# Optimization experiments

Hardware: AMD Instinct MI355X
Metric: run time of the kernel (lower is better)

## Reference

```python
import math
import jax, jax.numpy as jnp
import numpy as np
from jax import lax

EPS = 1e-6
SAMPLE_RATIO = 0.25
K = 5


def _grid_idx(loc_orig, h, w):
    # loc_orig in [-1,1] -> nearest grid cell flat index (row-major)
    loc = (jnp.clip(loc_orig, -1.0, 1.0) + 1.0) * 0.5
    col = jnp.clip(jnp.round(loc[..., 0] * (w - 1)).astype(jnp.int32), 0, w - 1)
    row = jnp.clip(jnp.round(loc[..., 1] * (h - 1)).astype(jnp.int32), 0, h - 1)
    return row * w + col


def token2map(x, loc_orig, idx_agg, H, W):
    # scatter tokens (via their original points) into an HxW grid, averaging per cell
    B, N, C = x.shape
    N0 = idx_agg.shape[1]
    idx_hw = _grid_idx(loc_orig, H, W)                      # (B, N0)
    tok = jax.vmap(lambda xb, ib: xb[ib])(x, idx_agg)       # (B, N0, C)

    def per_b(ihw, t):
        cnt = jax.ops.segment_sum(jnp.ones((N0,), x.dtype), ihw, num_segments=H * W)
        s = jax.ops.segment_sum(t, ihw, num_segments=H * W)
        return s / (cnt + EPS)[:, None]

    grid = jax.vmap(per_b)(idx_hw, tok)                     # (B, H*W, C)
    return grid.reshape(B, H, W, C).transpose(0, 3, 1, 2)   # (B, C, H, W)


def map2token(x_map, N, loc_orig, idx_agg, agg_weight):
    # gather map values at original points, weighted scatter-reduce back to N tokens
    B, C, h, w = x_map.shape
    idx_hw = _grid_idx(loc_orig, h, w)
    flat = x_map.reshape(B, C, h * w).transpose(0, 2, 1)    # (B, hw, C)
    feat = jax.vmap(lambda fb, ib: fb[ib])(flat, idx_hw)    # (B, N0, C)
    aw = agg_weight[..., 0]                                 # (B, N0)

    def per_b(ia, a, f):
        tot = jax.ops.segment_sum(a, ia, num_segments=N) + EPS
        return jax.ops.segment_sum(f * (a / tot[ia])[:, None], ia, num_segments=N)

    return jax.vmap(per_b)(idx_agg, aw, feat)               # (B, N, C)


def cluster_dpc_knn(x, cluster_num, k):
    # DPC-KNN: density from k-NN distances, parent distance, score = dist*density
    B, N, C = x.shape
    sq = jnp.sum(x * x, -1)
    dist = jnp.sqrt(jnp.maximum(sq[:, :, None] + sq[:, None, :]
                                - 2.0 * jnp.einsum('bnc,bmc->bnm', x, x), 0.0)) / math.sqrt(C)
    neg_near, _ = lax.top_k(-dist, k)                       # k nearest (incl. self, dist 0)
    density = jnp.exp(-jnp.mean(jnp.square(neg_near), -1))  # (B, N)
    mask = density[:, None, :] > density[:, :, None]
    dist_max = jnp.max(dist.reshape(B, -1), -1)[:, None, None]
    d_parent = jnp.min(jnp.where(mask, dist, dist_max), -1)
    score = d_parent * density
    _, index_down = lax.top_k(score, cluster_num)           # (B, M) cluster centers
    dist_down = jax.vmap(lambda db, ib: db[ib])(dist, index_down)  # (B, M, N)
    idx_cluster = jnp.argmin(dist_down, axis=1)             # (B, N)
    b = jnp.arange(B)[:, None]
    idx_cluster = idx_cluster.at[b, index_down].set(jnp.arange(cluster_num)[None, :])
    return idx_cluster


def layer_norm(x, g, b):
    mu = jnp.mean(x, -1, keepdims=True)
    xc = x - mu
    return xc * lax.rsqrt(jnp.mean(xc * xc, -1, keepdims=True) + 1e-5) * g + b


def setup_inputs() -> dict:
    key = jax.random.key(0)
    ks = jax.random.split(key, 8)
    B, N, C, DOUT, H, W = 4, 4096, 128, 256, 64, 64
    return {
        "x": jax.random.normal(ks[0], (B, N, C), jnp.float32),
        "loc_orig": jax.random.uniform(ks[1], (B, N, 2), jnp.float32, minval=-1.0, maxval=1.0),
        "idx_agg": jax.random.randint(ks[2], (B, N), 0, N),
        "agg_weight": jax.random.uniform(ks[3], (B, N, 1), jnp.float32),
        "H": H,
        "W": W,
        "idx_k_loc": jax.random.randint(ks[4], (B, N, K), 0, N),
        "conv_w": jax.random.normal(ks[5], (DOUT, C, 3, 3), jnp.float32) * 0.02,
        "conv_b": jnp.zeros((DOUT,), jnp.float32),
        "skip_w": jax.random.normal(ks[6], (DOUT, C), jnp.float32) * 0.02,
        "ln_g": jnp.ones((DOUT,), jnp.float32),
        "ln_b": jnp.zeros((DOUT,), jnp.float32),
        "conf_w": jax.random.normal(ks[7], (1, DOUT), jnp.float32) * 0.02,
        "conf_b": jnp.zeros((1,), jnp.float32),
    }


def reference(x, loc_orig, idx_agg, agg_weight, H, W, idx_k_loc,
              conv_w, conv_b, skip_w, ln_g, ln_b, conf_w, conf_b):
    B, N, C = x.shape
    x_map = token2map(x, loc_orig, idx_agg, H, W)           # (B, C, H, W)
    x_map = lax.conv_general_dilated(x_map, conv_w, (2, 2), ((1, 1), (1, 1)),
                                     dimension_numbers=('NCHW', 'OIHW', 'NCHW'))
    x_map = x_map + conv_b[None, :, None, None]             # (B, DOUT, H/2, W/2)
    xt = map2token(x_map, N, loc_orig, idx_agg, agg_weight) + x @ skip_w.T
    xt = layer_norm(xt, ln_g, ln_b)
    conf = xt @ conf_w.T + conf_b                           # (B, N, 1)
    weight = jnp.exp(conf)[..., 0]                          # (B, N)
    M = max(int(math.ceil(N * SAMPLE_RATIO)), 1)
    idx_cluster = cluster_dpc_knn(xt, M, K)                 # (B, N)

    def merge_b(ic, wb, xb):
        allw = jax.ops.segment_sum(wb, ic, num_segments=M) + EPS
        nw = wb / allw[ic]
        return jax.ops.segment_sum(xb * nw[:, None], ic, num_segments=M), nw

    x_down, norm_w = jax.vmap(merge_b)(idx_cluster, weight, xt)   # (B, M, DOUT), (B, N)
    idx_agg_down = jax.vmap(lambda ic, ia: ic[ia])(idx_cluster, idx_agg)        # (B, N0)
    weight_t = jax.vmap(lambda nw, ia: nw[ia])(norm_w, idx_agg)[..., None]      # (B, N0, 1)
    agg_weight_down = agg_weight * weight_t
    agg_weight_down = agg_weight_down / jnp.max(agg_weight_down, axis=1, keepdims=True)
    # down_block treated as identity (external module); use_grid=False path -> idx_k_loc_down is None
    return (x_down, idx_agg_down, agg_weight_down)
```

## Files before the change

kernel.cpp:

```cpp
#include <hip/hip_runtime.h>
#include <math.h>

#define NB 4
#define NT 4096
#define CI 128
#define DOUT 256
#define HWI 4096
#define HWO 1024
#define MC 1024
#define EPS_F 1e-6f
#define GSZ 16777216ull
#define GSZB 67108864ull

typedef unsigned short u16;
typedef __attribute__((ext_vector_type(8))) short bf16x8;
typedef __attribute__((ext_vector_type(4))) float f32x4;

static const size_t OFF_XMAP  = 0;
static const size_t OFF_CNT   = OFF_XMAP + 8388608;
static const size_t OFF_TOT   = OFF_CNT  + 65536;
static const size_t OFF_ALLW  = OFF_TOT  + 65536;
static const size_t OFF_VMAX  = OFF_ALLW + 16384;
static const size_t OFF_AWDM  = OFF_VMAX + 256;
static const size_t ZERO_BYTES= OFF_AWDM + 256;
static const size_t OFF_YMAP  = ZERO_BYTES;
static const size_t OFF_XT    = OFF_YMAP + 4194304;
static const size_t OFF_SQ    = OFF_XT + 16777216;
static const size_t OFF_DEN   = OFF_SQ + 65536;
static const size_t OFF_SCORE = OFF_DEN + 65536;
static const size_t OFF_WT    = OFF_SCORE + 65536;
static const size_t OFF_AWD   = OFF_WT + 65536;
static const size_t OFF_IDXD  = OFF_AWD + 65536;
static const size_t OFF_IDXC  = OFF_IDXD + 16384;
static const size_t OFF_INV   = OFF_IDXC + 65536;
static const size_t OFF_WTR   = OFF_INV + 65536;
static const size_t OFF_SWT   = OFF_WTR + 1179648;
static const size_t OFF_P     = OFF_SWT + 131072;
static const size_t OFF_XH    = OFF_P + 18874368;
static const size_t OFF_XM    = OFF_XH + 8388608;
static const size_t OFF_XL    = OFF_XM + 8388608;
static const size_t OFF_G     = OFF_XL + 8388608;
static const size_t DPSTRIDE  = (size_t)NT*32*6;

__device__ __forceinline__ float waveSum(float v){
#pragma unroll
  for (int m = 1; m < 64; m <<= 1) v += __shfl_xor(v, m, 64);
  return v;
}
__device__ __forceinline__ float blockSum256(float v, float* red){
  v = waveSum(v);
  int lane = threadIdx.x & 63, wid = threadIdx.x >> 6;
  __syncthreads();
  if (lane == 0) red[wid] = v;
  __syncthreads();
  return red[0] + red[1] + red[2] + red[3];
}
__device__ __forceinline__ void merge5(float& a0, float& a1, float& a2, float& a3, float& a4,
                                       float b0, float b1, float b2, float b3, float b4){
  float l0=a0,l1=a1,l2=a2,l3=fminf(a3,b4),l4=fminf(a4,b3),l5=b2,l6=b1,l7=b0;
  float t0=fminf(l0,l4), t4=fmaxf(l0,l4);
  float t1=fminf(l1,l5), t5=fmaxf(l1,l5);
  float t2=fminf(l2,l6), t6=fmaxf(l2,l6);
  float t3=fminf(l3,l7), t7=fmaxf(l3,l7);
  float u0=fminf(t0,t2), u2=fmaxf(t0,t2);
  float u1=fminf(t1,t3), u3=fmaxf(t1,t3);
  float u4=fminf(t4,t6);
  float u5=fminf(t5,t7);
  a0=fminf(u0,u1); a1=fmaxf(u0,u1);
  a2=fminf(u2,u3); a3=fmaxf(u2,u3);
  a4=fminf(u4,u5);
}
__device__ __forceinline__ void ins5(float v, float& t0, float& t1, float& t2, float& t3, float& t4){
  t4 = fminf(t4, v);
  float a;
  a = fminf(t3,t4); t4 = fmaxf(t3,t4); t3 = a;
  a = fminf(t2,t3); t3 = fmaxf(t2,t3); t2 = a;
  a = fminf(t1,t2); t2 = fmaxf(t1,t2); t1 = a;
  a = fminf(t0,t1); t1 = fmaxf(t0,t1); t0 = a;
}
__device__ __forceinline__ int grid_cell(float lx, float ly, int dim){
  lx = (fminf(fmaxf(lx, -1.f), 1.f) + 1.f) * 0.5f;
  ly = (fminf(fmaxf(ly, -1.f), 1.f) + 1.f) * 0.5f;
  float s = (float)(dim - 1);
  int col = (int)rintf(lx * s); col = min(max(col, 0), dim - 1);
  int row = (int)rintf(ly * s); row = min(max(row, 0), dim - 1);
  return row * dim + col;
}

__global__ __launch_bounds__(256) void t2m_scatter(const float* __restrict__ x,
                                                   const float* __restrict__ loc,
                                                   const int* __restrict__ idx_agg,
                                                   const float* __restrict__ aggw,
                                                   float* __restrict__ xmap, float* __restrict__ cnt,
                                                   float* __restrict__ tot){
  int lin = blockIdx.x * 256 + threadIdx.x;
// ... 128 lines not shown
  atomicAdd(&xt[((size_t)(b*NT + ia))*DOUT + d], val);
}

__global__ __launch_bounds__(256) void ln_kernel(float* __restrict__ xt,
                                                 const float* __restrict__ g,
                                                 const float* __restrict__ bta,
                                                 const float* __restrict__ cw,
                                                 const float* __restrict__ cb,
                                                 float* __restrict__ sq, float* __restrict__ wt){
  __shared__ float red[4];
  int row = blockIdx.x;
  int d = threadIdx.x;
  float v = xt[(size_t)row*DOUT + d];
  float mu = blockSum256(v, red) * (1.0f/256.0f);
  float xc = v - mu;
  float var = blockSum256(xc*xc, red) * (1.0f/256.0f);
  float rn = 1.0f / sqrtf(var + 1e-5f);
  float y = xc * rn * g[d] + bta[d];
  xt[(size_t)row*DOUT + d] = y;
  float s2 = blockSum256(y*y, red);
  float cf = blockSum256(y*cw[d], red);
  if (d == 0){ sq[row] = s2; wt[row] = expf(cf + cb[0]); }
}

__global__ __launch_bounds__(256) void xsplit_kernel(const float* __restrict__ xt,
                                                     u16* __restrict__ xh,
                                                     u16* __restrict__ xm,
                                                     u16* __restrict__ xl){
  int idx = blockIdx.x*256 + threadIdx.x;
  float2 v = *(const float2*)(xt + (size_t)idx*2);
  unsigned ph, pm, pl;
  {
    unsigned u = __float_as_uint(v.x);
    unsigned h0 = u >> 16;
    float r1 = v.x - __uint_as_float(u & 0xFFFF0000u);
    unsigned u1 = __float_as_uint(r1);
    unsigned m0 = u1 >> 16;
    float r2 = r1 - __uint_as_float(u1 & 0xFFFF0000u);
    unsigned l0 = __float_as_uint(r2) >> 16;
    unsigned u2 = __float_as_uint(v.y);
    unsigned h1 = u2 >> 16;
    float s1 = v.y - __uint_as_float(u2 & 0xFFFF0000u);
    unsigned u3 = __float_as_uint(s1);
    unsigned m1 = u3 >> 16;
    float s2 = s1 - __uint_as_float(u3 & 0xFFFF0000u);
    unsigned l1 = __float_as_uint(s2) >> 16;
    ph = h0 | (h1 << 16); pm = m0 | (m1 << 16); pl = l0 | (l1 << 16);
  }
  *(unsigned*)(xh + (size_t)idx*2) = ph;
  *(unsigned*)(xm + (size_t)idx*2) = pm;
  *(unsigned*)(xl + (size_t)idx*2) = pl;
}

__global__ __launch_bounds__(256) void gram_mfma(const u16* __restrict__ xh,
                                                 const u16* __restrict__ xm,
                                                 const u16* __restrict__ xl,
                                                 const float* __restrict__ sq,
                                                 float* __restrict__ G,
                                                 float* __restrict__ Dpart,
                                                 int b_base, size_t gstride){
  __shared__ u16 usmem[24576];
  u16* Au = usmem;
  u16* Bu = usmem + 12288;
  int b = b_base + blockIdx.y;
  float* Gb = G + (size_t)blockIdx.y*gstride;
  float* Dp = Dpart + (size_t)blockIdx.y*DPSTRIDE;
  int t = blockIdx.x;
  int ti = 0, accu = 0;
  while (accu + ti + 1 <= t){ accu += ti + 1; ++ti; }
  int tj = t - accu;
  int i0 = ti*128, j0 = tj*128;
  int tid = threadIdx.x;
  int w = tid >> 6, l = tid & 63;
  int lrow = l & 15, lg = l >> 4;
  int li = tid & 127, kq = tid >> 7;
  const size_t base = (size_t)b*NT*256;
  size_t arow = base + (size_t)(i0 + li)*256 + kq*16;
  size_t brow = base + (size_t)(j0 + li)*256 + kq*16;
  const u16* csrc[3] = {xh, xm, xl};
  int ga0 = ((li*4 + kq*2 + 0) ^ (li & 7)) * 8;
  int ga1 = ((li*4 + kq*2 + 1) ^ (li & 7)) * 8;
  f32x4 acc[2][8];
  f32x4 z; z[0]=0.f; z[1]=0.f; z[2]=0.f; z[3]=0.f;
#pragma unroll
  for (int mr = 0; mr < 2; ++mr)
#pragma unroll
    for (int n0 = 0; n0 < 8; ++n0) acc[mr][n0] = z;
  for (int kc = 0; kc < 8; ++kc){
    int k0 = kc*32;
    __syncthreads();
#pragma unroll
    for (int c = 0; c < 3; ++c){
      const u16* s = csrc[c];
      bf16x8 a0 = *(const bf16x8*)(s + arow + k0);
      bf16x8 a1 = *(const bf16x8*)(s + arow + k0 + 8);
      bf16x8 b0 = *(const bf16x8*)(s + brow + k0);
      bf16x8 b1 = *(const bf16x8*)(s + brow + k0 + 8);
      *(bf16x8*)(Au + c*4096 + ga0) = a0;
      *(bf16x8*)(Au + c*4096 + ga1) = a1;
      *(bf16x8*)(Bu + c*4096 + ga0) = b0;
      *(bf16x8*)(Bu + c*4096 + ga1) = b1;
    }
    __syncthreads();
    bf16x8 af[2][3];
#pragma unroll
    for (int mr = 0; mr < 2; ++mr){
      int row = w*32 + mr*16 + lrow;
      int off = ((row*4 + lg) ^ (row & 7)) * 8;
#pragma unroll
      for (int c = 0; c < 3; ++c)
        af[mr][c] = *(const bf16x8*)(Au + c*4096 + off);
    }
#pragma unroll
    for (int n0 = 0; n0 < 8; ++n0){
      int rowb = n0*16 + lrow;
      int offb = ((rowb*4 + lg) ^ (rowb & 7)) * 8;
      bf16x8 bh = *(const bf16x8*)(Bu + 0*4096 + offb);
      bf16x8 bm = *(const bf16x8*)(Bu + 1*4096 + offb);
      bf16x8 bl = *(const bf16x8*)(Bu + 2*4096 + offb);
#pragma unroll
      for (int mr = 0; mr < 2; ++mr){
        acc[mr][n0] = __builtin_amdgcn_mfma_f32_16x16x32_bf16(af[mr][0], bh, acc[mr][n0], 0, 0, 0);
        acc[mr][n0] = __builtin_amdgcn_mfma_f32_16x16x32_bf16(af[mr][0], bm, acc[mr][n0], 0, 0, 0);
        acc[mr][n0] = __builtin_amdgcn_mfma_f32_16x16x32_bf16(af[mr][1], bh, acc[mr][n0], 0, 0, 0);
        acc[mr][n0] = __builtin_amdgcn_mfma_f32_16x16x32_bf16(af[mr][1], bm, acc[mr][n0], 0, 0, 0);
        acc[mr][n0] = __builtin_amdgcn_mfma_f32_16x16x32_bf16(af[mr][0], bl, acc[mr][n0], 0, 0, 0);
        acc[mr][n0] = __builtin_amdgcn_mfma_f32_16x16x32_bf16(af[mr][2], bh, acc[mr][n0], 0, 0, 0);
      }
    }
  }
  const float* sqb2 = sq + b*NT;
  {
    float sqj_c[8];
#pragma unroll
    for (int n0 = 0; n0 < 8; ++n0) sqj_c[n0] = sqb2[j0 + n0*16 + lrow];
#pragma unroll
    for (int mr = 0; mr < 2; ++mr)
#pragma unroll
      for (int r = 0; r < 4; ++r){
        int row = i0 + w*32 + mr*16 + lg*4 + r;
        float sqi_v = sqb2[row];
        float t0=INFINITY,t1=INFINITY,t2=INFINITY,t3=INFINITY,t4=INFINITY;
        float mx = 0.f;
#pragma unroll
        for (int n0 = 0; n0 < 8; ++n0){
          float v = fmaxf(sqi_v + sqj_c[n0] - 2.0f*acc[mr][n0][r], 0.0f);
          mx = fmaxf(mx, v);
          ins5(v,t0,t1,t2,t3,t4);
        }
#pragma unroll
        for (int m = 1; m < 16; m <<= 1){
          float b0=__shfl_xor(t0,m,64), b1=__shfl_xor(t1,m,64), b2=__shfl_xor(t2,m,64),
                b3=__shfl_xor(t3,m,64), b4=__shfl_xor(t4,m,64);
          merge5(t0,t1,t2,t3,t4,b0,b1,b2,b3,b4);
          mx = fmaxf(mx, __shfl_xor(mx,m,64));
        }
        if (lrow == 0){
          float* dpp = Dp + ((size_t)row*32 + tj)*6;
          dpp[0]=t0; dpp[1]=t1; dpp[2]=t2; dpp[3]=t3; dpp[4]=t4; dpp[5]=mx;
        }
      }
  }
#pragma unroll
  for (int mr = 0; mr < 2; ++mr)
#pragma unroll
    for (int n0 = 0; n0 < 8; ++n0)
#pragma unroll
      for (int r = 0; r < 4; ++r)
        Gb[(size_t)(i0 + w*32 + mr*16 + lg*4 + r)*NT + j0 + n0*16 + lrow] = acc[mr][n0][r];
  if (ti != tj){
    float* T = (float*)usmem;
    int q = tid >> 3, u = tid & 7;
    float sqi_u[16];
#pragma unroll
    for (int e = 0; e < 16; ++e) sqi_u[e] = sqb2[i0 + u*16 + e];
#pragma unroll
    for (int cc = 0; cc < 4; ++cc){
      __syncthreads();
#pragma unroll
      for (int nn = 0; nn < 2; ++nn){
        int n0 = cc*2 + nn;
#pragma unroll
        for (int mr = 0; mr < 2; ++mr)
#pragma unroll
          for (int r = 0; r < 4; ++r)
            T[(nn*16 + lrow)*129 + w*32 + mr*16 + lg*4 + r] = acc[mr][n0][r];
      }
      __syncthreads();
      const float* Trow = &T[q*129 + u*16];
      float* dst = Gb + (size_t)(j0 + cc*32 + q)*NT + i0 + u*16;
      float gv[16];
#pragma unroll
      for (int e = 0; e < 16; ++e) gv[e] = Trow[e];
      float4 o0, o1, o2, o3;
      o0.x=gv[0]; o0.y=gv[1]; o0.z=gv[2]; o0.w=gv[3];
      o1.x=gv[4]; o1.y=gv[5]; o1.z=gv[6]; o1.w=gv[7];
      o2.x=gv[8]; o2.y=gv[9]; o2.z=gv[10]; o2.w=gv[11];
      o3.x=gv[12]; o3.y=gv[13]; o3.z=gv[14]; o3.w=gv[15];
      *(float4*)dst = o0; *(float4*)(dst + 4) = o1;
      *(float4*)(dst + 8) = o2; *(float4*)(dst + 12) = o3;
      {
        int jr = j0 + cc*32 + q;
        float sqj_m = sqb2[jr];
        float t0=INFINITY,t1=INFINITY,t2=INFINITY,t3=INFINITY,t4=INFINITY;
        float mx = 0.f;
#pragma unroll
        for (int e = 0; e < 16; ++e){
          float v = fmaxf(sqj_m + sqi_u[e] - 2.0f*gv[e], 0.0f);
          mx = fmaxf(mx, v);
          ins5(v,t0,t1,t2,t3,t4);
        }
#pragma unroll
        for (int m = 1; m < 8; m <<= 1){
          float b0=__shfl_xor(t0,m,64), b1=__shfl_xor(t1,m,64), b2=__shfl_xor(t2,m,64),
                b3=__shfl_xor(t3,m,64), b4=__shfl_xor(t4,m,64);
          merge5(t0,t1,t2,t3,t4,b0,b1,b2,b3,b4);
          mx = fmaxf(mx, __shfl_xor(mx,m,64));
        }
        if (u == 0){
          float* dpp = Dp + ((size_t)jr*32 + ti)*6;
          dpp[0]=t0; dpp[1]=t1; dpp[2]=t2; dpp[3]=t3; dpp[4]=t4; dpp[5]=mx;
        }
      }
    }
  }
}

__global__ __launch_bounds__(256) void dens_merge(const float* __restrict__ Dpart,
                                                  float* __restrict__ density, int* __restrict__ vmax,
                                                  int b_base){
  int b = b_base + blockIdx.y;
  const float* Dp = Dpart + (size_t)blockIdx.y*DPSTRIDE;
  int row = blockIdx.x*256 + threadIdx.x;
  const float* p = Dp + (size_t)row*32*6;
  float t0=INFINITY,t1=INFINITY,t2=INFINITY,t3=INFINITY,t4=INFINITY;
  float mx = 0.f;
#pragma unroll 4
  for (int tt = 0; tt < 32; ++tt){
    merge5(t0,t1,t2,t3,t4, p[tt*6+0], p[tt*6+1], p[tt*6+2], p[tt*6+3], p[tt*6+4]);
    mx = fmaxf(mx, p[tt*6+5]);
  }
  float d0=sqrtf(t0)*0.0625f, d1=sqrtf(t1)*0.0625f, d2=sqrtf(t2)*0.0625f,
        d3=sqrtf(t3)*0.0625f, d4=sqrtf(t4)*0.0625f;
  float s = d0*d0; s += d1*d1; s += d2*d2; s += d3*d3; s += d4*d4;
  density[b*NT + row] = expf(-(s / 5.0f));
#pragma unroll
  for (int m = 1; m < 64; m <<= 1) mx = fmaxf(mx, __shfl_xor(mx, m, 64));
  if ((threadIdx.x & 63) == 0) atomicMax(vmax + b, __float_as_int(mx));
}

__global__ __launch_bounds__(256) void parent_all(const float* __restrict__ G, size_t gstride,
                                                  const float* __restrict__ sq,
                                                  const float* __restrict__ density, const int* __restrict__ vmax,
                                                  float* __restrict__ score, int b_base){
  int b = b_base + blockIdx.y;
  const float* Gb = G + (size_t)blockIdx.y*gstride;
  int i = blockIdx.x*4 + (threadIdx.x >> 6);
  int lane = threadIdx.x & 63;
  const float* sqb = sq + b*NT;
  const float* den = density + b*NT;
  float sqi = sqb[i];
  float di = den[i];
  const float4* row4 = (const float4*)(Gb + (size_t)i*NT);
  const float4* sq4  = (const float4*)sqb;
  const float4* dn4  = (const float4*)den;
  float4 ga[8], gb2[8];
#pragma unroll
  for (int p = 0; p < 8; ++p) ga[p] = row4[p*64 + lane];
#pragma unroll
  for (int p = 0; p < 8; ++p) gb2[p] = row4[(8+p)*64 + lane];
  float minv = INFINITY;
#pragma unroll
  for (int p = 0; p < 8; ++p){
    float4 g4 = ga[p];
    float4 s4 = sq4[p*64 + lane];
    float4 d4 = dn4[p*64 + lane];
    float v0 = fmaxf(sqi + s4.x - 2.0f*g4.x, 0.0f);
    float v1 = fmaxf(sqi + s4.y - 2.0f*g4.y, 0.0f);
    float v2 = fmaxf(sqi + s4.z - 2.0f*g4.z, 0.0f);
    float v3 = fmaxf(sqi + s4.w - 2.0f*g4.w, 0.0f);
    minv = fminf(minv, (d4.x > di) ? v0 : INFINITY);
    minv = fminf(minv, (d4.y > di) ? v1 : INFINITY);
    minv = fminf(minv, (d4.z > di) ? v2 : INFINITY);
    minv = fminf(minv, (d4.w > di) ? v3 : INFINITY);
  }
#pragma unroll
  for (int p = 0; p < 8; ++p){
    float4 g4 = gb2[p];
    float4 s4 = sq4[(8+p)*64 + lane];
    float4 d4 = dn4[(8+p)*64 + lane];
    float v0 = fmaxf(sqi + s4.x - 2.0f*g4.x, 0.0f);
    float v1 = fmaxf(sqi + s4.y - 2.0f*g4.y, 0.0f);
    float v2 = fmaxf(sqi + s4.z - 2.0f*g4.z, 0.0f);
    float v3 = fmaxf(sqi + s4.w - 2.0f*g4.w, 0.0f);
    minv = fminf(minv, (d4.x > di) ? v0 : INFINITY);
    minv = fminf(minv, (d4.y > di) ? v1 : INFINITY);
    minv = fminf(minv, (d4.z > di) ? v2 : INFINITY);
    minv = fminf(minv, (d4.w > di) ? v3 : INFINITY);
  }
#pragma unroll
  for (int m = 1; m < 64; m <<= 1) minv = fminf(minv, __shfl_xor(minv,m,64));
  if (lane == 0){
    float dmax = sqrtf(__int_as_float(vmax[b])) * 0.0625f;
    float dp = isinf(minv) ? dmax : sqrtf(minv) * 0.0625f;
    score[b*NT + i] = dp * di;
  }
}

__device__ __forceinline__ bool kv_lt(float s1, int a1, float s2, int a2){
  return (s1 > s2) || (s1 == s2 && a1 < a2);
}
#define KV_CMPX(sx,ax,sy,ay,up) do{ bool _l = kv_lt(sx,ax,sy,ay); \
  if (_l != (up)) { float _ts=sx; sx=sy; sy=_ts; int _ta=ax; ax=ay; ay=_ta; } }while(0)
#define KV_TAKE(sx,ax,ps,pa,eqd) do{ bool _keep = kv_lt(sx,ax,ps,pa) == (eqd); \
  if(!_keep){ sx=(ps); ax=(pa); } }while(0)

__global__ __launch_bounds__(1024) void topk_all(const float* __restrict__ score, int* __restrict__ idx_down,
                                                 int* __restrict__ inv, int b_base){
  __shared__ float ss[4096];
  __shared__ int ii[4096];
  int b = b_base + blockIdx.x;
  int t = threadIdx.x;
  float s0,s1,s2,s3; int a0,a1,a2,a3;
  {
    float4 v = *(const float4*)(score + b*NT + 4*t);
    s0=v.x; s1=v.y; s2=v.z; s3=v.w;
    a0=4*t; a1=4*t+1; a2=4*t+2; a3=4*t+3;
    int4 mi; mi.x=-1; mi.y=-1; mi.z=-1; mi.w=-1;
    *(int4*)(inv + b*NT + 4*t) = mi;
  }
  for (int k = 2; k <= 4096; k <<= 1){
    bool upT = ((4*t) & k) == 0;
    for (int j = k >> 1; j >= 256; j >>= 1){
      __syncthreads();
      float4 sv; sv.x=s0; sv.y=s1; sv.z=s2; sv.w=s3;
      int4 av; av.x=a0; av.y=a1; av.z=a2; av.w=a3;
      *(float4*)&ss[4*t] = sv;
      *(int4*)&ii[4*t] = av;
      __syncthreads();
      int pt = t ^ (j >> 2);
      bool eqd = ((t & (j >> 2)) == 0) == upT;
      float4 ps = *(const float4*)&ss[4*pt];
      int4  pa = *(const int4*)&ii[4*pt];
      KV_TAKE(s0,a0,ps.x,pa.x,eqd);
      KV_TAKE(s1,a1,ps.y,pa.y,eqd);
      KV_TAKE(s2,a2,ps.z,pa.z,eqd);
      KV_TAKE(s3,a3,ps.w,pa.w,eqd);
    }
    int jhi = (k >> 1) < 128 ? (k >> 1) : 128;
    for (int j = jhi; j >= 4; j >>= 1){
      int dl = j >> 2;
      bool eqd = ((t & dl) == 0) == upT;
      { float ps=__shfl_xor(s0,dl,64); int pa=__shfl_xor(a0,dl,64); KV_TAKE(s0,a0,ps,pa,eqd); }
      { float ps=__shfl_xor(s1,dl,64); int pa=__shfl_xor(a1,dl,64); KV_TAKE(s1,a1,ps,pa,eqd); }
      { float ps=__shfl_xor(s2,dl,64); int pa=__shfl_xor(a2,dl,64); KV_TAKE(s2,a2,ps,pa,eqd); }
      { float ps=__shfl_xor(s3,dl,64); int pa=__shfl_xor(a3,dl,64); KV_TAKE(s3,a3,ps,pa,eqd); }
    }
    if (k >= 4){
      KV_CMPX(s0,a0,s2,a2,upT);
      KV_CMPX(s1,a1,s3,a3,upT);
      KV_CMPX(s0,a0,s1,a1,upT);
      KV_CMPX(s2,a2,s3,a3,upT);
    } else {
      KV_CMPX(s0,a0,s1,a1,true);
      KV_CMPX(s2,a2,s3,a3,false);
    }
  }
  __syncthreads();
  if (t < 256){
    idx_down[b*MC + 4*t + 0] = a0; inv[b*NT + a0] = 4*t + 0;
    idx_down[b*MC + 4*t + 1] = a1; inv[b*NT + a1] = 4*t + 1;
    idx_down[b*MC + 4*t + 2] = a2; inv[b*NT + a2] = 4*t + 2;
    idx_down[b*MC + 4*t + 3] = a3; inv[b*NT + a3] = 4*t + 3;
  }
}

__global__ __launch_bounds__(256) void assign_all(const float* __restrict__ G, size_t gstride,
                                                  const float* __restrict__ sq,
                                                  const int* __restrict__ idx_down, const int* __restrict__ inv,
                                                  const float* __restrict__ wt,
                                                  int* __restrict__ idx_cluster, float* __restrict__ allw,
                                                  int b_base){
  int b = b_base + blockIdx.y;
  const float* Gb = G + (size_t)blockIdx.y*gstride;
  int jl = threadIdx.x & 15, mq = threadIdx.x >> 4;
  int j = blockIdx.x * 16 + jl;
  const float* sqb = sq + b*NT;
  float sqj = sqb[j];
  const int* idb = idx_down + b*MC;
  float bestd = INFINITY; int bestm = 0x7fffffff;
  for (int m = mq*64; m < mq*64 + 64; ++m){
    int im = idb[m];
    float g = Gb[(size_t)im*NT + j];
    float v = fmaxf(sqb[im] + sqj - 2.0f*g, 0.0f);
    float d = sqrtf(v) * 0.0625f;
    if (d < bestd){ bestd = d; bestm = m; }
  }
  __shared__ float ld[16][17];
  __shared__ int lm[16][17];
  ld[mq][jl] = bestd; lm[mq][jl] = bestm;
  __syncthreads();
  if (mq == 0){
    for (int q = 1; q < 16; ++q){
      float d2 = ld[q][jl]; int m2 = lm[q][jl];
      if (d2 < bestd || (d2 == bestd && m2 < bestm)){ bestd = d2; bestm = m2; }
    }
    int iv = inv[b*NT + j];
    int final_m = (iv >= 0) ? iv : bestm;
    idx_cluster[b*NT + j] = final_m;
    atomicAdd(&allw[b*MC + final_m], wt[b*NT + j]);
  }
}

__global__ __launch_bounds__(256) void xdown_kernel(const int* __restrict__ idx_cluster,
                                                    const float* __restrict__ wt, const float* __restrict__ allw,
                                                    const float* __restrict__ xt, float* __restrict__ out0){
  int bn = blockIdx.x;
  int d = threadIdx.x;
  int b = bn >> 12;
  int ic = idx_cluster[bn];
  float nw = wt[bn] / (allw[b*MC + ic] + EPS_F);
  float v = xt[(size_t)bn*DOUT + d] * nw;
  atomicAdd(&out0[((size_t)(b*MC + ic))*DOUT + d], v);
}
__global__ __launch_bounds__(256) void out12a_kernel(const int* __restrict__ idx_agg, const int* __restrict__ idx_cluster,
                                                     const float* __restrict__ aggw,
                                                     const float* __restrict__ wt, const float* __restrict__ allw,
                                                     float* __restrict__ awd, int* __restrict__ awdmax,
                                                     float* __restrict__ out1){
  __shared__ float red[4];
  int lin = blockIdx.x * 256 + threadIdx.x;
  int b = lin >> 12;
  int ia = idx_agg[lin];
  int ic = idx_cluster[b*NT + ia];
  out1[lin] = (float)ic;
  float nw = wt[b*NT + ia] / (allw[b*MC + ic] + EPS_F);
  float v = aggw[lin] * nw;
  awd[lin] = v;
  float wv = v;
#pragma unroll
  for (int m = 1; m < 64; m <<= 1) wv = fmaxf(wv, __shfl_xor(wv, m, 64));
  int lane = threadIdx.x & 63, wid = threadIdx.x >> 6;
  if (lane == 0) red[wid] = wv;
  __syncthreads();
  if (threadIdx.x == 0){
    float bm = fmaxf(fmaxf(red[0], red[1]), fmaxf(red[2], red[3]));
    atomicMax(&awdmax[b], __float_as_int(bm));
  }
}
__global__ __launch_bounds__(256) void out2_kernel(const float* __restrict__ awd, const int* __restrict__ awdmax,
                                                   float* __restrict__ out2){
  int lin = blockIdx.x * 256 + threadIdx.x;
  int b = lin >> 12;
  out2[lin] = awd[lin] / __int_as_float(awdmax[b]);
}

extern "C" void kernel_launch(void* const* d_in, const int* in_sizes, int n_in,
                              void* d_out, int out_size, void* d_ws, size_t ws_size,
                              hipStream_t stream) {
  const float* x      = (const float*)d_in[0];
  const float* loc    = (const float*)d_in[1];
  const int*   idxagg = (const int*)d_in[2];
  const float* aggw   = (const float*)d_in[3];
  const float* convw  = (const float*)d_in[7];
  const float* convb  = (const float*)d_in[8];
  const float* skipw  = (const float*)d_in[9];
  const float* lng    = (const float*)d_in[10];
  const float* lnb    = (const float*)d_in[11];
  const float* confw  = (const float*)d_in[12];
  const float* confb  = (const float*)d_in[13];

  char* ws = (char*)d_ws;
  float* w_xmap  = (float*)(ws + OFF_XMAP);
  float* w_cnt   = (float*)(ws + OFF_CNT);
  float* w_tot   = (float*)(ws + OFF_TOT);
  float* w_allw  = (float*)(ws + OFF_ALLW);
  int*   w_vmax  = (int*)  (ws + OFF_VMAX);
  int*   w_awdm  = (int*)  (ws + OFF_AWDM);
  float* w_ymap  = (float*)(ws + OFF_YMAP);
  float* w_xt    = (float*)(ws + OFF_XT);
  float* w_sq    = (float*)(ws + OFF_SQ);
  float* w_den   = (float*)(ws + OFF_DEN);
  float* w_score = (float*)(ws + OFF_SCORE);
  float* w_wt    = (float*)(ws + OFF_WT);
  float* w_awd   = (float*)(ws + OFF_AWD);
  int*   w_idxd  = (int*)  (ws + OFF_IDXD);
  int*   w_idxc  = (int*)  (ws + OFF_IDXC);
  int*   w_inv   = (int*)  (ws + OFF_INV);
  float* w_wtr   = (float*)(ws + OFF_WTR);
  float* w_swt   = (float*)(ws + OFF_SWT);
  float* w_p     = (float*)(ws + OFF_P);
  u16*   w_xh    = (u16*)  (ws + OFF_XH);
  u16*   w_xm    = (u16*)  (ws + OFF_XM);
  u16*   w_xl    = (u16*)  (ws + OFF_XL);
  float* w_g     = (float*)(ws + OFF_G);
  float* w_dpart = (float*)(ws + OFF_P);

  int gcount = 1;
  for (int k = 4; k >= 1; --k){
    if (OFF_G + (size_t)k*GSZB <= ws_size){ gcount = k; break; }
  }

  float* out0 = (float*)d_out;
  float* out1 = out0 + NB*MC*DOUT;
  float* out2 = out1 + NB*NT;

  hipMemsetAsync(ws, 0, ZERO_BYTES, stream);
  hipMemsetAsync(out0, 0, (size_t)NB*MC*DOUT*sizeof(float), stream);

  t2m_scatter<<<NB*NT*CI/256, 256, 0, stream>>>(x, loc, idxagg, aggw, w_xmap, w_cnt, w_tot);
  wprep_kernel<<<1280, 256, 0, stream>>>(convw, skipw, w_wtr, w_swt);
  im2col_kernel<<<2048, 256, 0, stream>>>(w_xmap, w_cnt, w_p);
  conv_gemm<<<dim3(64, 8), 256, 0, stream>>>(w_p, w_wtr, convb, w_ymap);
  skip_kernel<<<NB*NT/8, 256, 0, stream>>>(x, w_swt, w_xt);
  m2t_scatter<<<NB*NT, 256, 0, stream>>>(w_ymap, loc, idxagg, aggw, w_tot, w_xt);
  ln_kernel<<<NB*NT, 256, 0, stream>>>(w_xt, lng, lnb, confw, confb, w_sq, w_wt);
  xsplit_kernel<<<NB*NT*DOUT/512, 256, 0, stream>>>(w_xt, w_xh, w_xm, w_xl);

  for (int g0 = 0; g0 < NB; g0 += gcount){
    int gy = (NB - g0 < gcount) ? (NB - g0) : gcount;
    gram_mfma  <<<dim3(528, gy), 256, 0, stream>>>(w_xh, w_xm, w_xl, w_sq, w_g, w_dpart, g0, GSZ);
    dens_merge <<<dim3(16, gy), 256, 0, stream>>>(w_dpart, w_den, w_vmax, g0);
    parent_all <<<dim3(1024, gy), 256, 0, stream>>>(w_g, GSZ, w_sq, w_den, w_vmax, w_score, g0);
    topk_all   <<<gy, 1024, 0, stream>>>(w_score, w_idxd, w_inv, g0);
    assign_all <<<dim3(256, gy), 256, 0, stream>>>(w_g, GSZ, w_sq, w_idxd, w_inv, w_wt, w_idxc, w_allw, g0);
  }

  xdown_kernel<<<NB*NT, 256, 0, stream>>>(w_idxc, w_wt, w_allw, w_xt, out0);
  out12a_kernel<<<NB*NT/256, 256, 0, stream>>>(idxagg, w_idxc, aggw, w_wt, w_allw, w_awd, w_awdm, out1);
  out2_kernel<<<NB*NT/256, 256, 0, stream>>>(w_awd, w_awdm, out2);

  (void)in_sizes; (void)n_in; (void)out_size;
}
```

Before: 635.0 us.

## Recompute Gram tiles via MFMA instead of materializing full distance matrix

Drops the stored 4096x4096 Gram matrix per batch. The parent-distance and cluster-assignment stages now recompute the needed dot products with split-bf16 MFMA tiles and reduce partial minima in small merge kernels. This removes the large writes and re-reads of the Gram matrix and the batch-group loop, and all batches launch in one grid. The cost is running the 3-way split MFMA gram about twice more (full for parent, 1024x4096 for assign).

```diff
diff --git a/kernel.cpp b/kernel.cpp
--- a/kernel.cpp
+++ b/kernel.cpp
@@ -9,8 +9,6 @@
 #define HWO 1024
 #define MC 1024
 #define EPS_F 1e-6f
-#define GSZ 16777216ull
-#define GSZB 67108864ull
 
 typedef unsigned short u16;
 typedef __attribute__((ext_vector_type(8))) short bf16x8;
@@ -39,8 +37,11 @@
 static const size_t OFF_XH    = OFF_P + 18874368;
 static const size_t OFF_XM    = OFF_XH + 8388608;
 static const size_t OFF_XL    = OFF_XM + 8388608;
-static const size_t OFF_G     = OFF_XL + 8388608;
+static const size_t OFF_PP    = OFF_XL + 8388608;
+static const size_t OFF_APD   = OFF_PP + (size_t)NB*NT*32*4;
+static const size_t OFF_APM   = OFF_APD + (size_t)NB*NT*8*4;
 static const size_t DPSTRIDE  = (size_t)NT*32*6;
+static const size_t PPSTRIDE  = (size_t)NT*32;
 
 __device__ __forceinline__ float waveSum(float v){
 #pragma unroll
@@ -275,19 +276,16 @@
   *(unsigned*)(xl + (size_t)idx*2) = pl;
 }
 
-__global__ __launch_bounds__(256) void gram_mfma(const u16* __restrict__ xh,
+__global__ __launch_bounds__(256) void dens_mfma(const u16* __restrict__ xh,
                                                  const u16* __restrict__ xm,
                                                  const u16* __restrict__ xl,
                                                  const float* __restrict__ sq,
-                                                 float* __restrict__ G,
-                                                 float* __restrict__ Dpart,
-                                                 int b_base, size_t gstride){
+                                                 float* __restrict__ Dpart){
   __shared__ u16 usmem[24576];
   u16* Au = usmem;
   u16* Bu = usmem + 12288;
-  int b = b_base + blockIdx.y;
-  float* Gb = G + (size_t)blockIdx.y*gstride;
-  float* Dp = Dpart + (size_t)blockIdx.y*DPSTRIDE;
+  int b = blockIdx.y;
+  float* Dp = Dpart + (size_t)b*DPSTRIDE;
   int t = blockIdx.x;
   int ti = 0, accu = 0;
   while (accu + ti + 1 <= t){ accu += ti + 1; ++ti; }
@@ -384,13 +382,6 @@
         }
       }
   }
-#pragma unroll
-  for (int mr = 0; mr < 2; ++mr)
-#pragma unroll
-    for (int n0 = 0; n0 < 8; ++n0)
-#pragma unroll
-      for (int r = 0; r < 4; ++r)
-        Gb[(size_t)(i0 + w*32 + mr*16 + lg*4 + r)*NT + j0 + n0*16 + lrow] = acc[mr][n0][r];
   if (ti != tj){
     float* T = (float*)usmem;
     int q = tid >> 3, u = tid & 7;
@@ -411,49 +402,38 @@
       }
       __syncthreads();
       const float* Trow = &T[q*129 + u*16];
-      float* dst = Gb + (size_t)(j0 + cc*32 + q)*NT + i0 + u*16;
       float gv[16];
 #pragma unroll
       for (int e = 0; e < 16; ++e) gv[e] = Trow[e];
-      float4 o0, o1, o2, o3;
-      o0.x=gv[0]; o0.y=gv[1]; o0.z=gv[2]; o0.w=gv[3];
-      o1.x=gv[4]; o1.y=gv[5]; o1.z=gv[6]; o1.w=gv[7];
-      o2.x=gv[8]; o2.y=gv[9]; o2.z=gv[10]; o2.w=gv[11];
-      o3.x=gv[12]; o3.y=gv[13]; o3.z=gv[14]; o3.w=gv[15];
-      *(float4*)dst = o0; *(float4*)(dst + 4) = o1;
-      *(float4*)(dst + 8) = o2; *(float4*)(dst + 12) = o3;
-      {
-        int jr = j0 + cc*32 + q;
-        float sqj_m = sqb2[jr];
-        float t0=INFINITY,t1=INFINITY,t2=INFINITY,t3=INFINITY,t4=INFINITY;
-        float mx = 0.f;
-#pragma unroll
-        for (int e = 0; e < 16; ++e){
-          float v = fmaxf(sqj_m + sqi_u[e] - 2.0f*gv[e], 0.0f);
-          mx = fmaxf(mx, v);
-          ins5(v,t0,t1,t2,t3,t4);
-        }
-#pragma unroll
-        for (int m = 1; m < 8; m <<= 1){
-          float b0=__shfl_xor(t0,m,64), b1=__shfl_xor(t1,m,64), b2=__shfl_xor(t2,m,64),
-                b3=__shfl_xor(t3,m,64), b4=__shfl_xor(t4,m,64);
-          merge5(t0,t1,t2,t3,t4,b0,b1,b2,b3,b4);
-          mx = fmaxf(mx, __shfl_xor(mx,m,64));
-        }
-        if (u == 0){
-          float* dpp = Dp + ((size_t)jr*32 + ti)*6;
-          dpp[0]=t0; dpp[1]=t1; dpp[2]=t2; dpp[3]=t3; dpp[4]=t4; dpp[5]=mx;
-        }
+      int jr = j0 + cc*32 + q;
+      float sqj_m = sqb2[jr];
+      float t0=INFINITY,t1=INFINITY,t2=INFINITY,t3=INFINITY,t4=INFINITY;
+      float mx = 0.f;
+#pragma unroll
+      for (int e = 0; e < 16; ++e){
+        float v = fmaxf(sqj_m + sqi_u[e] - 2.0f*gv[e], 0.0f);
+        mx = fmaxf(mx, v);
+        ins5(v,t0,t1,t2,t3,t4);
+      }
+#pragma unroll
+      for (int m = 1; m < 8; m <<= 1){
+        float b0=__shfl_xor(t0,m,64), b1=__shfl_xor(t1,m,64), b2=__shfl_xor(t2,m,64),
+              b3=__shfl_xor(t3,m,64), b4=__shfl_xor(t4,m,64);
+        merge5(t0,t1,t2,t3,t4,b0,b1,b2,b3,b4);
+        mx = fmaxf(mx, __shfl_xor(mx,m,64));
+      }
+      if (u == 0){
+        float* dpp = Dp + ((size_t)jr*32 + ti)*6;
+        dpp[0]=t0; dpp[1]=t1; dpp[2]=t2; dpp[3]=t3; dpp[4]=t4; dpp[5]=mx;
       }
     }
   }
 }
 
 __global__ __launch_bounds__(256) void dens_merge(const float* __restrict__ Dpart,
-                                                  float* __restrict__ density, int* __restrict__ vmax,
-                                                  int b_base){
-  int b = b_base + blockIdx.y;
-  const float* Dp = Dpart + (size_t)blockIdx.y*DPSTRIDE;
+                                                  float* __restrict__ density, int* __restrict__ vmax){
+  int b = blockIdx.y;
+  const float* Dp = Dpart + (size_t)b*DPSTRIDE;
   int row = blockIdx.x*256 + threadIdx.x;
   const float* p = Dp + (size_t)row*32*6;
   float t0=INFINITY,t1=INFINITY,t2=INFINITY,t3=INFINITY,t4=INFINITY;
@@ -472,62 +452,160 @@
   if ((threadIdx.x & 63) == 0) atomicMax(vmax + b, __float_as_int(mx));
 }
 
-__global__ __launch_bounds__(256) void parent_all(const float* __restrict__ G, size_t gstride,
-                                                  const float* __restrict__ sq,
-                                                  const float* __restrict__ density, const int* __restrict__ vmax,
-                                                  float* __restrict__ score, int b_base){
-  int b = b_base + blockIdx.y;
-  const float* Gb = G + (size_t)blockIdx.y*gstride;
-  int i = blockIdx.x*4 + (threadIdx.x >> 6);
-  int lane = threadIdx.x & 63;
-  const float* sqb = sq + b*NT;
-  const float* den = density + b*NT;
-  float sqi = sqb[i];
-  float di = den[i];
-  const float4* row4 = (const float4*)(Gb + (size_t)i*NT);
-  const float4* sq4  = (const float4*)sqb;
-  const float4* dn4  = (const float4*)den;
-  float4 ga[8], gb2[8];
-#pragma unroll
-  for (int p = 0; p < 8; ++p) ga[p] = row4[p*64 + lane];
-#pragma unroll
-  for (int p = 0; p < 8; ++p) gb2[p] = row4[(8+p)*64 + lane];
-  float minv = INFINITY;
-#pragma unroll
-  for (int p = 0; p < 8; ++p){
-    float4 g4 = ga[p];
-    float4 s4 = sq4[p*64 + lane];
-    float4 d4 = dn4[p*64 + lane];
-    float v0 = fmaxf(sqi + s4.x - 2.0f*g4.x, 0.0f);
-    float v1 = fmaxf(sqi + s4.y - 2.0f*g4.y, 0.0f);
-    float v2 = fmaxf(sqi + s4.z - 2.0f*g4.z, 0.0f);
-    float v3 = fmaxf(sqi + s4.w - 2.0f*g4.w, 0.0f);
-    minv = fminf(minv, (d4.x > di) ? v0 : INFINITY);
-    minv = fminf(minv, (d4.y > di) ? v1 : INFINITY);
-    minv = fminf(minv, (d4.z > di) ? v2 : INFINITY);
-    minv = fminf(minv, (d4.w > di) ? v3 : INFINITY);
-  }
-#pragma unroll
-  for (int p = 0; p < 8; ++p){
-    float4 g4 = gb2[p];
-    float4 s4 = sq4[(8+p)*64 + lane];
-    float4 d4 = dn4[(8+p)*64 + lane];
-    float v0 = fmaxf(sqi + s4.x - 2.0f*g4.x, 0.0f);
-    float v1 = fmaxf(sqi + s4.y - 2.0f*g4.y, 0.0f);
-    float v2 = fmaxf(sqi + s4.z - 2.0f*g4.z, 0.0f);
-    float v3 = fmaxf(sqi + s4.w - 2.0f*g4.w, 0.0f);
-    minv = fminf(minv, (d4.x > di) ? v0 : INFINITY);
-    minv = fminf(minv, (d4.y > di) ? v1 : INFINITY);
-    minv = fminf(minv, (d4.z > di) ? v2 : INFINITY);
-    minv = fminf(minv, (d4.w > di) ? v3 : INFINITY);
-  }
-#pragma unroll
-  for (int m = 1; m < 64; m <<= 1) minv = fminf(minv, __shfl_xor(minv,m,64));
-  if (lane == 0){
-    float dmax = sqrtf(__int_as_float(vmax[b])) * 0.0625f;
-    float dp = isinf(minv) ? dmax : sqrtf(minv) * 0.0625f;
-    score[b*NT + i] = dp * di;
-  }
+__global__ __launch_bounds__(256) void parent_mfma(const u16* __restrict__ xh,
+                                                   const u16* __restrict__ xm,
+                                                   const u16* __restrict__ xl,
+                                                   const float* __restrict__ sq,
+                                                   const float* __restrict__ den,
+                                                   float* __restrict__ Ppart){
+  __shared__ u16 usmem[24576];
+  u16* Au = usmem;
+  u16* Bu = usmem + 12288;
+  int b = blockIdx.y;
+  float* Pp = Ppart + (size_t)b*PPSTRIDE;
+  int t = blockIdx.x;
+  int ti = 0, accu = 0;
+  while (accu + ti + 1 <= t){ accu += ti + 1; ++ti; }
+  int tj = t - accu;
+  int i0 = ti*128, j0 = tj*128;
+  int tid = threadIdx.x;
+  int w = tid >> 6, l = tid & 63;
+  int lrow = l & 15, lg = l >> 4;
+  int li = tid & 127, kq = tid >> 7;
+  const size_t base = (size_t)b*NT*256;
+  size_t arow = base + (size_t)(i0 + li)*256 + kq*16;
+  size_t brow = base + (size_t)(j0 + li)*256 + kq*16;
+  const u16* csrc[3] = {xh, xm, xl};
+  int ga0 = ((li*4 + kq*2 + 0) ^ (li & 7)) * 8;
+  int ga1 = ((li*4 + kq*2 + 1) ^ (li & 7)) * 8;
+  f32x4 acc[2][8];
+  f32x4 z; z[0]=0.f; z[1]=0.f; z[2]=0.f; z[3]=0.f;
+#pragma unroll
+  for (int mr = 0; mr < 2; ++mr)
+#pragma unroll
+    for (int n0 = 0; n0 < 8; ++n0) acc[mr][n0] = z;
+  for (int kc = 0; kc < 8; ++kc){
+    int k0 = kc*32;
+    __syncthreads();
+#pragma unroll
+    for (int c = 0; c < 3; ++c){
+      const u16* s = csrc[c];
+      bf16x8 a0 = *(const bf16x8*)(s + arow + k0);
+      bf16x8 a1 = *(const bf16x8*)(s + arow + k0 + 8);
+      bf16x8 b0 = *(const bf16x8*)(s + brow + k0);
+      bf16x8 b1 = *(const bf16x8*)(s + brow + k0 + 8);
+      *(bf16x8*)(Au + c*4096 + ga0) = a0;
+      *(bf16x8*)(Au + c*4096 + ga1) = a1;
+      *(bf16x8*)(Bu + c*4096 + ga0) = b0;
+      *(bf16x8*)(Bu + c*4096 + ga1) = b1;
+    }
+    __syncthreads();
+    bf16x8 af[2][3];
+#pragma unroll
+    for (int mr = 0; mr < 2; ++mr){
+      int row = w*32 + mr*16 + lrow;
+      int off = ((row*4 + lg) ^ (row & 7)) * 8;
+#pragma unroll
+      for (int c = 0; c < 3; ++c)
+        af[mr][c] = *(const bf16x8*)(Au + c*4096 + off);
+    }
+#pragma unroll
+    for (int n0 = 0; n0 < 8; ++n0){
+      int rowb = n0*16 + lrow;
+      int offb = ((rowb*4 + lg) ^ (rowb & 7)) * 8;
+      bf16x8 bh = *(const bf16x8*)(Bu + 0*4096 + offb);
+      bf16x8 bm = *(const bf16x8*)(Bu + 1*4096 + offb);
+      bf16x8 bl = *(const bf16x8*)(Bu + 2*4096 + offb);
+#pragma unroll
+      for (int mr = 0; mr < 2; ++mr){
+        acc[mr][n0] = __builtin_amdgcn_mfma_f32_16x16x32_bf16(af[mr][0], bh, acc[mr][n0], 0, 0, 0);
+        acc[mr][n0] = __builtin_amdgcn_mfma_f32_16x16x32_bf16(af[mr][0], bm, acc[mr][n0], 0, 0, 0);
+        acc[mr][n0] = __builtin_amdgcn_mfma_f32_16x16x32_bf16(af[mr][1], bh, acc[mr][n0], 0, 0, 0);
+        acc[mr][n0] = __builtin_amdgcn_mfma_f32_16x16x32_bf16(af[mr][1], bm, acc[mr][n0], 0, 0, 0);
+        acc[mr][n0] = __builtin_amdgcn_mfma_f32_16x16x32_bf16(af[mr][0], bl, acc[mr][n0], 0, 0, 0);
+        acc[mr][n0] = __builtin_amdgcn_mfma_f32_16x16x32_bf16(af[mr][2], bh, acc[mr][n0], 0, 0, 0);
+      }
+    }
+  }
+  const float* sqb2 = sq + b*NT;
+  const float* denb = den + b*NT;
+  {
+    float sqj_c[8], dnj_c[8];
+#pragma unroll
+    for (int n0 = 0; n0 < 8; ++n0){
+      sqj_c[n0] = sqb2[j0 + n0*16 + lrow];
+      dnj_c[n0] = denb[j0 + n0*16 + lrow];
+    }
+#pragma unroll
+    for (int mr = 0; mr < 2; ++mr)
+#pragma unroll
+      for (int r = 0; r < 4; ++r){
+        int row = i0 + w*32 + mr*16 + lg*4 + r;
+        float di = denb[row];
+        float sqi_v = sqb2[row];
+        float mn = INFINITY;
+#pragma unroll
+        for (int n0 = 0; n0 < 8; ++n0){
+          float v = fmaxf(sqi_v + sqj_c[n0] - 2.0f*acc[mr][n0][r], 0.0f);
+          mn = fminf(mn, (dnj_c[n0] > di) ? v : INFINITY);
+        }
+#pragma unroll
+        for (int m = 1; m < 16; m <<= 1) mn = fminf(mn, __shfl_xor(mn, m, 64));
+        if (lrow == 0) Pp[(size_t)row*32 + tj] = mn;
+      }
+  }
+  if (ti != tj){
+    float* T = (float*)usmem;
+    int q = tid >> 3, u = tid & 7;
+    float sqi_u[16], dni_u[16];
+#pragma unroll
+    for (int e = 0; e < 16; ++e){
+      sqi_u[e] = sqb2[i0 + u*16 + e];
+      dni_u[e] = denb[i0 + u*16 + e];
+    }
+#pragma unroll
+    for (int cc = 0; cc < 4; ++cc){
+      __syncthreads();
+#pragma unroll
+      for (int nn = 0; nn < 2; ++nn){
+        int n0 = cc*2 + nn;
+#pragma unroll
+        for (int mr = 0; mr < 2; ++mr)
+#pragma unroll
+          for (int r = 0; r < 4; ++r)
+            T[(nn*16 + lrow)*129 + w*32 + mr*16 + lg*4 + r] = acc[mr][n0][r];
+      }
+      __syncthreads();
+      const float* Trow = &T[q*129 + u*16];
+      int jr = j0 + cc*32 + q;
+      float dj = denb[jr];
+      float sqj_m = sqb2[jr];
+      float mn = INFINITY;
+#pragma unroll
+      for (int e = 0; e < 16; ++e){
+        float v = fmaxf(sqj_m + sqi_u[e] - 2.0f*Trow[e], 0.0f);
+        mn = fminf(mn, (dni_u[e] > dj) ? v : INFINITY);
+      }
+#pragma unroll
+      for (int m = 1; m < 8; m <<= 1) mn = fminf(mn, __shfl_xor(mn, m, 64));
+      if (u == 0) Pp[(size_t)jr*32 + ti] = mn;
+    }
+  }
+}
+
+__global__ __launch_bounds__(256) void parent_merge(const float* __restrict__ Ppart,
+                                                    const float* __restrict__ density,
+                                                    const int* __restrict__ vmax,
+                                                    float* __restrict__ score){
+  int b = blockIdx.y;
+  int row = blockIdx.x*256 + threadIdx.x;
+  const float* p = Ppart + (size_t)b*PPSTRIDE + (size_t)row*32;
+  float mn = INFINITY;
+#pragma unroll 4
+  for (int tt = 0; tt < 32; ++tt) mn = fminf(mn, p[tt]);
+  float dmax = sqrtf(__int_as_float(vmax[b])) * 0.0625f;
+  float dp = isinf(mn) ? dmax : sqrtf(mn) * 0.0625f;
+  score[b*NT + row] = dp * density[b*NT + row];
 }
 
 __device__ __forceinline__ bool kv_lt(float s1, int a1, float s2, int a2){
@@ -539,10 +617,10 @@
   if(!_keep){ sx=(ps); ax=(pa); } }while(0)
 
 __global__ __launch_bounds__(1024) void topk_all(const float* __restrict__ score, int* __restrict__ idx_down,
-                                                 int* __restrict__ inv, int b_base){
+                                                 int* __restrict__ inv){
   __shared__ float ss[4096];
   __shared__ int ii[4096];
-  int b = b_base + blockIdx.x;
+  int b = blockIdx.x;
   int t = threadIdx.x;
   float s0,s1,s2,s3; int a0,a1,a2,a3;
   {
@@ -598,41 +676,150 @@
   }
 }
 
-__global__ __launch_bounds__(256) void assign_all(const float* __restrict__ G, size_t gstride,
-                                                  const float* __restrict__ sq,
-                                                  const int* __restrict__ idx_down, const int* __restrict__ inv,
-                                                  const float* __restrict__ wt,
-                                                  int* __restrict__ idx_cluster, float* __restrict__ allw,
-                                                  int b_base){
-  int b = b_base + blockIdx.y;
-  const float* Gb = G + (size_t)blockIdx.y*gstride;
-  int jl = threadIdx.x & 15, mq = threadIdx.x >> 4;
-  int j = blockIdx.x * 16 + jl;
-  const float* sqb = sq + b*NT;
-  float sqj = sqb[j];
-  const int* idb = idx_down + b*MC;
-  float bestd = INFINITY; int bestm = 0x7fffffff;
-  for (int m = mq*64; m < mq*64 + 64; ++m){
-    int im = idb[m];
-    float g = Gb[(size_t)im*NT + j];
-    float v = fmaxf(sqb[im] + sqj - 2.0f*g, 0.0f);
-    float d = sqrtf(v) * 0.0625f;
-    if (d < bestd){ bestd = d; bestm = m; }
-  }
-  __shared__ float ld[16][17];
-  __shared__ int lm[16][17];
-  ld[mq][jl] = bestd; lm[mq][jl] = bestm;
+__global__ __launch_bounds__(256) void assign_mfma(const u16* __restrict__ xh,
+                                                   const u16* __restrict__ xm,
+                                                   const u16* __restrict__ xl,
+                                                   const float* __restrict__ sq,
+                                                   const int* __restrict__ idx_down,
+                                                   float* __restrict__ Apd, int* __restrict__ Apm){
+  __shared__ u16 usmem[24576];
+  __shared__ int idbs[128];
+  u16* Au = usmem;
+  u16* Bu = usmem + 12288;
+  int b = blockIdx.y;
+  int ct = blockIdx.x >> 5;
+  int jt = blockIdx.x & 31;
+  int j0 = jt*128;
+  int tid = threadIdx.x;
+  int w = tid >> 6, l = tid & 63;
+  int lrow = l & 15, lg = l >> 4;
+  int li = tid & 127, kq = tid >> 7;
+  if (tid < 128) idbs[tid] = idx_down[b*MC + ct*128 + tid];
   __syncthreads();
-  if (mq == 0){
-    for (int q = 1; q < 16; ++q){
-      float d2 = ld[q][jl]; int m2 = lm[q][jl];
-      if (d2 < bestd || (d2 == bestd && m2 < bestm)){ bestd = d2; bestm = m2; }
-    }
-    int iv = inv[b*NT + j];
-    int final_m = (iv >= 0) ? iv : bestm;
-    idx_cluster[b*NT + j] = final_m;
-    atomicAdd(&allw[b*MC + final_m], wt[b*NT + j]);
-  }
+  const size_t base = (size_t)b*NT*256;
+  size_t arow = base + (size_t)idbs[li]*256 + kq*16;
+  size_t brow = base + (size_t)(j0 + li)*256 + kq*16;
+  const u16* csrc[3] = {xh, xm, xl};
+  int ga0 = ((li*4 + kq*2 + 0) ^ (li & 7)) * 8;
+  int ga1 = ((li*4 + kq*2 + 1) ^ (li & 7)) * 8;
+  f32x4 acc[2][8];
+  f32x4 z; z[0]=0.f; z[1]=0.f; z[2]=0.f; z[3]=0.f;
+#pragma unroll
+  for (int mr = 0; mr < 2; ++mr)
+#pragma unroll
+    for (int n0 = 0; n0 < 8; ++n0) acc[mr][n0] = z;
+  for (int kc = 0; kc < 8; ++kc){
+    int k0 = kc*32;
+    __syncthreads();
+#pragma unroll
+    for (int c = 0; c < 3; ++c){
+      const u16* s = csrc[c];
+      bf16x8 a0 = *(const bf16x8*)(s + arow + k0);
+      bf16x8 a1 = *(const bf16x8*)(s + arow + k0 + 8);
+      bf16x8 b0 = *(const bf16x8*)(s + brow + k0);
+      bf16x8 b1 = *(const bf16x8*)(s + brow + k0 + 8);
+      *(bf16x8*)(Au + c*4096 + ga0) = a0;
+      *(bf16x8*)(Au + c*4096 + ga1) = a1;
+      *(bf16x8*)(Bu + c*4096 + ga0) = b0;
+      *(bf16x8*)(Bu + c*4096 + ga1) = b1;
+    }
+    __syncthreads();
+    bf16x8 af[2][3];
+#pragma unroll
+    for (int mr = 0; mr < 2; ++mr){
+      int row = w*32 + mr*16 + lrow;
+      int off = ((row*4 + lg) ^ (row & 7)) * 8;
+#pragma unroll
+      for (int c = 0; c < 3; ++c)
+        af[mr][c] = *(const bf16x8*)(Au + c*4096 + off);
+    }
+#pragma unroll
+    for (int n0 = 0; n0 < 8; ++n0){
+      int rowb = n0*16 + lrow;
+      int offb = ((rowb*4 + lg) ^ (rowb & 7)) * 8;
+      bf16x8 bh = *(const bf16x8*)(Bu + 0*4096 + offb);
+      bf16x8 bm = *(const bf16x8*)(Bu + 1*4096 + offb);
+      bf16x8 bl = *(const bf16x8*)(Bu + 2*4096 + offb);
+#pragma unroll
+      for (int mr = 0; mr < 2; ++mr){
+        acc[mr][n0] = __builtin_amdgcn_mfma_f32_16x16x32_bf16(af[mr][0], bh, acc[mr][n0], 0, 0, 0);
+        acc[mr][n0] = __builtin_amdgcn_mfma_f32_16x16x32_bf16(af[mr][0], bm, acc[mr][n0], 0, 0, 0);
+        acc[mr][n0] = __builtin_amdgcn_mfma_f32_16x16x32_bf16(af[mr][1], bh, acc[mr][n0], 0, 0, 0);
+        acc[mr][n0] = __builtin_amdgcn_mfma_f32_16x16x32_bf16(af[mr][1], bm, acc[mr][n0], 0, 0, 0);
+        acc[mr][n0] = __builtin_amdgcn_mfma_f32_16x16x32_bf16(af[mr][0], bl, acc[mr][n0], 0, 0, 0);
+        acc[mr][n0] = __builtin_amdgcn_mfma_f32_16x16x32_bf16(af[mr][2], bh, acc[mr][n0], 0, 0, 0);
+      }
+    }
+  }
+  const float* sqb2 = sq + b*NT;
+  float sqj_c[8];
+#pragma unroll
+  for (int n0 = 0; n0 < 8; ++n0) sqj_c[n0] = sqb2[j0 + n0*16 + lrow];
+  float bd[8]; int bm2[8];
+#pragma unroll
+  for (int n0 = 0; n0 < 8; ++n0){ bd[n0] = INFINITY; bm2[n0] = 0x7fffffff; }
+#pragma unroll
+  for (int mr = 0; mr < 2; ++mr)
+#pragma unroll
+    for (int r = 0; r < 4; ++r){
+      int ml = w*32 + mr*16 + lg*4 + r;
+      float sqi_v = sqb2[idbs[ml]];
+#pragma unroll
+      for (int n0 = 0; n0 < 8; ++n0){
+        float v = fmaxf(sqi_v + sqj_c[n0] - 2.0f*acc[mr][n0][r], 0.0f);
+        float d = sqrtf(v) * 0.0625f;
+        if (d < bd[n0] || (d == bd[n0] && ml < bm2[n0])){ bd[n0] = d; bm2[n0] = ml; }
+      }
+    }
+#pragma unroll
+  for (int m = 16; m < 64; m <<= 1)
+#pragma unroll
+    for (int n0 = 0; n0 < 8; ++n0){
+      float od = __shfl_xor(bd[n0], m, 64);
+      int   om = __shfl_xor(bm2[n0], m, 64);
+      if (od < bd[n0] || (od == bd[n0] && om < bm2[n0])){ bd[n0] = od; bm2[n0] = om; }
+    }
+  __syncthreads();
+  float* sd = (float*)usmem;
+  int*   sm = (int*)(usmem + 1024);
+  if (lg == 0){
+#pragma unroll
+    for (int n0 = 0; n0 < 8; ++n0){
+      sd[w*128 + n0*16 + lrow] = bd[n0];
+      sm[w*128 + n0*16 + lrow] = bm2[n0];
+    }
+  }
+  __syncthreads();
+  if (tid < 128){
+    float d = sd[tid]; int m = sm[tid];
+#pragma unroll
+    for (int ww = 1; ww < 4; ++ww){
+      float od = sd[ww*128 + tid]; int om = sm[ww*128 + tid];
+      if (od < d || (od == d && om < m)){ d = od; m = om; }
+    }
+    int j = j0 + tid;
+    Apd[((size_t)b*NT + j)*8 + ct] = d;
+    Apm[((size_t)b*NT + j)*8 + ct] = ct*128 + m;
+  }
+}
+
+__global__ __launch_bounds__(256) void assign_merge(const float* __restrict__ Apd, const int* __restrict__ Apm,
+                                                    const int* __restrict__ inv, const float* __restrict__ wt,
+                                                    int* __restrict__ idx_cluster, float* __restrict__ allw){
+  int b = blockIdx.y;
+  int j = blockIdx.x*256 + threadIdx.x;
+  const float* pd = Apd + ((size_t)b*NT + j)*8;
+  const int*   pm = Apm + ((size_t)b*NT + j)*8;
+  float bdv = INFINITY; int bmv = 0x7fffffff;
+#pragma unroll
+  for (int ct = 0; ct < 8; ++ct){
+    float d = pd[ct]; int m = pm[ct];
+    if (d < bdv || (d == bdv && m < bmv)){ bdv = d; bmv = m; }
+  }
+  int iv = inv[b*NT + j];
+  int fm = (iv >= 0) ? iv : bmv;
+  idx_cluster[b*NT + j] = fm;
+  atomicAdd(&allw[b*MC + fm], wt[b*NT + j]);
 }
 
 __global__ __launch_bounds__(256) void xdown_kernel(const int* __restrict__ idx_cluster,
@@ -716,13 +903,10 @@
   u16*   w_xh    = (u16*)  (ws + OFF_XH);
   u16*   w_xm    = (u16*)  (ws + OFF_XM);
   u16*   w_xl    = (u16*)  (ws + OFF_XL);
-  float* w_g     = (float*)(ws + OFF_G);
   float* w_dpart = (float*)(ws + OFF_P);
-
-  int gcount = 1;
-  for (int k = 4; k >= 1; --k){
-    if (OFF_G + (size_t)k*GSZB <= ws_size){ gcount = k; break; }
-  }
+  float* w_ppart = (float*)(ws + OFF_PP);
+  float* w_apd   = (float*)(ws + OFF_APD);
+  int*   w_apm   = (int*)  (ws + OFF_APM);
 
   float* out0 = (float*)d_out;
   float* out1 = out0 + NB*MC*DOUT;
@@ -740,18 +924,17 @@
   ln_kernel<<<NB*NT, 256, 0, stream>>>(w_xt, lng, lnb, confw, confb, w_sq, w_wt);
   xsplit_kernel<<<NB*NT*DOUT/512, 256, 0, stream>>>(w_xt, w_xh, w_xm, w_xl);
 
-  for (int g0 = 0; g0 < NB; g0 += gcount){
-    int gy = (NB - g0 < gcount) ? (NB - g0) : gcount;
-    gram_mfma  <<<dim3(528, gy), 256, 0, stream>>>(w_xh, w_xm, w_xl, w_sq, w_g, w_dpart, g0, GSZ);
-    dens_merge <<<dim3(16, gy), 256, 0, stream>>>(w_dpart, w_den, w_vmax, g0);
-    parent_all <<<dim3(1024, gy), 256, 0, stream>>>(w_g, GSZ, w_sq, w_den, w_vmax, w_score, g0);
-    topk_all   <<<gy, 1024, 0, stream>>>(w_score, w_idxd, w_inv, g0);
-    assign_all <<<dim3(256, gy), 256, 0, stream>>>(w_g, GSZ, w_sq, w_idxd, w_inv, w_wt, w_idxc, w_allw, g0);
-  }
+  dens_mfma   <<<dim3(528, NB), 256, 0, stream>>>(w_xh, w_xm, w_xl, w_sq, w_dpart);
+  dens_merge  <<<dim3(16, NB), 256, 0, stream>>>(w_dpart, w_den, w_vmax);
+  parent_mfma <<<dim3(528, NB), 256, 0, stream>>>(w_xh, w_xm, w_xl, w_sq, w_den, w_ppart);
+  parent_merge<<<dim3(16, NB), 256, 0, stream>>>(w_ppart, w_den, w_vmax, w_score);
+  topk_all    <<<NB, 1024, 0, stream>>>(w_score, w_idxd, w_inv);
+  assign_mfma <<<dim3(256, NB), 256, 0, stream>>>(w_xh, w_xm, w_xl, w_sq, w_idxd, w_apd, w_apm);
+  assign_merge<<<dim3(16, NB), 256, 0, stream>>>(w_apd, w_apm, w_inv, w_wt, w_idxc, w_allw);
 
   xdown_kernel<<<NB*NT, 256, 0, stream>>>(w_idxc, w_wt, w_allw, w_xt, out0);
   out12a_kernel<<<NB*NT/256, 256, 0, stream>>>(idxagg, w_idxc, aggw, w_wt, w_allw, w_awd, w_awdm, out1);
   out2_kernel<<<NB*NT/256, 256, 0, stream>>>(w_awd, w_awdm, out2);
 
-  (void)in_sizes; (void)n_in; (void)out_size;
-}
+  (void)in_sizes; (void)n_in; (void)out_size; (void)ws_size;
+}
```

After: 692.5 us. 1.09x slower.
